# Kernel tuning notes

Hardware: AMD Instinct MI355X
Metric: run time of the kernel (lower is better)

Reference implementation:

```python
import jax, jax.numpy as jnp
import numpy as np

B, N, D = 1, 768, 256
H = 4
HD = D // H
K = 16
EDGE_DIM = 4
LN_EPS = 1e-5


def setup_inputs() -> dict:
    key = jax.random.key(0)
    ks = jax.random.split(key, 16)
    g = lambda k, shape, fan: jax.random.normal(k, shape, jnp.float32) / np.sqrt(fan)
    return {
        'x': jax.random.normal(ks[0], (B, N, D), jnp.float32),
        'Wqkv_w': g(ks[1], (D, 3 * D), D), 'Wqkv_b': jnp.zeros((3 * D,), jnp.float32),
        'out_w': g(ks[2], (D, D), D), 'out_b': jnp.zeros((D,), jnp.float32),
        'ffn1_w': g(ks[3], (2 * D, 2 * D), 2 * D), 'ffn1_b': jnp.zeros((2 * D,), jnp.float32),
        'ln_g': jnp.ones((2 * D,), jnp.float32), 'ln_b': jnp.zeros((2 * D,), jnp.float32),
        'ffn2_w': g(ks[4], (2 * D, D), 2 * D), 'ffn2_b': jnp.zeros((D,), jnp.float32),
        'e1_w': g(ks[5], (EDGE_DIM, 2 * H), EDGE_DIM), 'e1_b': jnp.zeros((2 * H,), jnp.float32),
        'e2_w': g(ks[6], (2 * H, H), 2 * H), 'e2_b': jnp.zeros((H,), jnp.float32),
        'graph_gate': jnp.float32(0.5),
    }


def _normalize(v):
    return v / jnp.clip(jnp.linalg.norm(v, axis=-1, keepdims=True), 1e-12)


def reference(x, Wqkv_w, Wqkv_b, out_w, out_b, ffn1_w, ffn1_b, ln_g, ln_b,
              ffn2_w, ffn2_b, e1_w, e1_b, e2_w, e2_b, graph_gate):
    b, n, d = x.shape
    # ---- graph topology (no grad, discrete top-k) ----
    xs = jax.lax.stop_gradient(x)
    dn_s = _normalize(xs)
    sim_d = jnp.einsum('bnd,bmd->bnm', dn_s, dn_s)
    eye = jnp.eye(n, dtype=bool)
    sim_d = jnp.where(eye, -jnp.inf, sim_d)
    idx = jax.lax.top_k(sim_d, K)[1]                       # (B,N,K)
    adj = jnp.zeros((b, n, n), bool).at[
        jnp.arange(b)[:, None, None], jnp.arange(n)[None, :, None], idx].set(True)
    adj = adj | jnp.swapaxes(adj, 1, 2) | eye              # symmetric + self loops
    # ---- differentiable edge features (B,N,N,4) ----
    dnm = _normalize(x)
    sim = jnp.einsum('bnd,bmd->bnm', dnm, dnm)
    diff = x[:, :, None, :] - x[:, None, :, :]             # (B,N,N,D) memory-bound
    l2 = jnp.linalg.norm(diff, axis=-1) / np.float32(np.sqrt(d))
    ad = jnp.abs(diff)
    ef = jnp.stack([sim, l2, ad.mean(-1), ad.max(-1)], axis=-1)
    # ---- edge bias per head (B,H,N,N) ----
    h = jax.nn.relu(ef @ e1_w + e1_b)
    bias = jnp.transpose(h @ e2_w + e2_b, (0, 3, 1, 2))
    # ---- attention ----
    qkv = (x @ Wqkv_w + Wqkv_b).reshape(b, n, H, HD, 3)
    qkv = jnp.transpose(qkv, (0, 2, 1, 3, 4))              # (B,H,N,HD,3)
    q, k, v = qkv[..., 0], qkv[..., 1], qkv[..., 2]
    logits = jnp.einsum('bhnd,bhmd->bhnm', q, k) / np.float32(np.sqrt(HD))
    logits = logits + graph_gate * bias
    logits = jnp.where(adj[:, None], logits, -jnp.inf)     # sparse masking
    attn = jax.nn.softmax(logits, axis=-1)
    ctx = jnp.einsum('bhnm,bhmd->bhnd', attn, v)
    msg = jnp.transpose(ctx, (0, 2, 1, 3)).reshape(b, n, d) @ out_w + out_b
    # ---- FFN: Linear -> LayerNorm -> GELU -> Linear, residual ----
    y = jnp.concatenate([x, msg], axis=-1) @ ffn1_w + ffn1_b
    mu = y.mean(-1, keepdims=True)
    var = ((y - mu) ** 2).mean(-1, keepdims=True)
    y = (y - mu) / jnp.sqrt(var + LN_EPS) * ln_g + ln_b
    y = jax.nn.gelu(y, approximate=False)
    return x + (y @ ffn2_w + ffn2_b)
```

## Files before the change

### kernel.cpp

```cpp
#include <hip/hip_runtime.h>
#include <hip/hip_bf16.h>
#include <math.h>

#define NN 768
#define DD 256
#define NHEAD 4
#define HDIM 64
#define TOPK 16

typedef __attribute__((ext_vector_type(8))) short short8;
typedef __attribute__((ext_vector_type(4))) float f32x4;

__device__ __forceinline__ unsigned short f2bf(float f) {
    unsigned u = __float_as_uint(f);
    unsigned r = u + 0x7fffu + ((u >> 16) & 1u);
    return (unsigned short)(r >> 16);
}

__global__ __launch_bounds__(256) void k_prep_norms(
        const float* __restrict__ Wqkv, const float* __restrict__ outw,
        const float* __restrict__ f1w,  const float* __restrict__ f2w,
        unsigned short* __restrict__ t_qkv, unsigned short* __restrict__ t_out,
        unsigned short* __restrict__ t_f1,  unsigned short* __restrict__ t_f2,
        const float* __restrict__ x,
        double* __restrict__ nrm2_d, double* __restrict__ nrm_d,
        double* __restrict__ invn_d,
        unsigned short* __restrict__ xb, unsigned int* __restrict__ adjw) {
    int b = blockIdx.x;
    int tid = threadIdx.x;
    if (b < 640) {
        const float* src; unsigned short* dst; int K, C, tile;
        if (b < 192)      { src = Wqkv; dst = t_qkv; K = 256; C = 768; tile = b; }
        else if (b < 256) { src = outw; dst = t_out; K = 256; C = 256; tile = b - 192; }
        else if (b < 512) { src = f1w;  dst = t_f1;  K = 512; C = 512; tile = b - 256; }
        else              { src = f2w;  dst = t_f2;  K = 512; C = 256; tile = b - 512; }
        int tpr = C / 32;
        int k0 = (tile / tpr) * 32, c0 = (tile % tpr) * 32;
        __shared__ float tls[32][33];
        int r = tid >> 3, c4 = (tid & 7) * 4;
        float4 v = *(const float4*)&src[(size_t)(k0 + r) * C + c0 + c4];
        tls[r][c4 + 0] = v.x; tls[r][c4 + 1] = v.y;
        tls[r][c4 + 2] = v.z; tls[r][c4 + 3] = v.w;
        __syncthreads();
        int rc = tid >> 3, k4 = (tid & 7) * 4;
        unsigned short* d = &dst[(size_t)(c0 + rc) * K + k0 + k4];
        d[0] = f2bf(tls[k4 + 0][rc]);
        d[1] = f2bf(tls[k4 + 1][rc]);
        d[2] = f2bf(tls[k4 + 2][rc]);
        d[3] = f2bf(tls[k4 + 3][rc]);
    } else {
        int nb = b - 640;
        int gid = nb * 256 + tid;
        adjw[gid * 3 + 0] = 0u;
        adjw[gid * 3 + 1] = 0u;
        adjw[gid * 3 + 2] = 0u;
        int n = nb * 4 + (tid >> 6);
        int lane = tid & 63;
        const float* row = x + (size_t)n * DD;
        double s = 0.0;
        #pragma unroll
        for (int i = 0; i < 4; ++i) {
            float v = row[lane + 64 * i];
            xb[(size_t)n * DD + lane + 64 * i] = f2bf(v);
            s += (double)v * (double)v;
        }
        for (int off = 32; off > 0; off >>= 1) s += __shfl_down(s, off);
        if (lane == 0) {
            nrm2_d[n] = s;
            double nv = sqrt(s);
            nrm_d[n] = nv;
            invn_d[n] = 1.0 / fmax(nv, 1e-12);
        }
    }
}

__global__ __launch_bounds__(512) void k_simqkv(
        const float* __restrict__ x, const double* __restrict__ invn_d,
        double* __restrict__ simd,
        const unsigned short* __restrict__ xbf,
        const unsigned short* __restrict__ t_qkv,
        const float* __restrict__ Wqkv_b,
        float* __restrict__ qb, float* __restrict__ kb, float* __restrict__ vb) {
    __shared__ float A[2][32][68];
    __shared__ float Bm[2][32][68];
    int b = blockIdx.x;
    int tid = threadIdx.x;
    if (b < 300) {
        int r = (int)((sqrtf(8.f * (float)b + 1.f) - 1.f) * 0.5f);
        while ((r + 1) * (r + 2) / 2 <= b) ++r;
        while (r * (r + 1) / 2 > b) --r;
        int c = b - r * (r + 1) / 2;
        int n0 = c * 32, m0 = r * 32;

        int g = tid >> 8;
        int t = tid & 255;
        int tx = t & 15, ty = t >> 4;
        double d00 = 0.0, d01 = 0.0, d10 = 0.0, d11 = 0.0;

        #pragma unroll
        for (int kt = 0; kt < 2; ++kt) {
            int d0 = g * 128 + kt * 64;
            #pragma unroll
            for (int it = 0; it < 8; ++it) {
                int l = t + 256 * it;
                int rr = l >> 6, cc = l & 63;
                A[g][rr][cc]  = x[(size_t)(n0 + rr) * DD + d0 + cc];
                Bm[g][rr][cc] = x[(size_t)(m0 + rr) * DD + d0 + cc];
            }
            __syncthreads();
            for (int d = 0; d < 64; d += 4) {
                float4 b0 = *(const float4*)&Bm[g][tx][d];
                float4 b1 = *(const float4*)&Bm[g][tx + 16][d];
                float4 a0 = *(const float4*)&A[g][ty][d];
                float4 a1 = *(const float4*)&A[g][ty + 16][d];
                double b0x = b0.x, b0y = b0.y, b0z = b0.z, b0w = b0.w;
                double b1x = b1.x, b1y = b1.y, b1z = b1.z, b1w = b1.w;
                double a0x = a0.x, a0y = a0.y, a0z = a0.z, a0w = a0.w;
                double a1x = a1.x, a1y = a1.y, a1z = a1.z, a1w = a1.w;
                d00 += a0x * b0x + a0y * b0y + a0z * b0z + a0w * b0w;
                d01 += a0x * b1x + a0y * b1y + a0z * b1z + a0w * b1w;
                d10 += a1x * b0x + a1y * b0y + a1z * b0z + a1w * b0w;
                d11 += a1x * b1x + a1y * b1y + a1z * b1z + a1w * b1w;
            }
            __syncthreads();
        }

        double* part = (double*)&A[0][0][0];
        if (g == 1) {
            part[t * 4 + 0] = d00; part[t * 4 + 1] = d01;
            part[t * 4 + 2] = d10; part[t * 4 + 3] = d11;
        }
        __syncthreads();
        if (g == 0) {
            d00 += part[t * 4 + 0]; d01 += part[t * 4 + 1];
            d10 += part[t * 4 + 2]; d11 += part[t * 4 + 3];
            double in_m0 = invn_d[m0 + tx], in_m1 = invn_d[m0 + tx + 16];
            double in_n0 = invn_d[n0 + ty], in_n1 = invn_d[n0 + ty + 16];
            double v00 = d00 * in_n0 * in_m0;
            double v01 = d01 * in_n0 * in_m1;
            double v10 = d10 * in_n1 * in_m0;
            double v11 = d11 * in_n1 * in_m1;
            simd[(size_t)(n0 + ty) * NN + m0 + tx]           = v00;
            simd[(size_t)(n0 + ty) * NN + m0 + tx + 16]      = v01;
            simd[(size_t)(n0 + ty + 16) * NN + m0 + tx]      = v10;
            simd[(size_t)(n0 + ty + 16) * NN + m0 + tx + 16] = v11;
            simd[(size_t)(m0 + tx) * NN + n0 + ty]           = v00;
            simd[(size_t)(m0 + tx + 16) * NN + n0 + ty]      = v01;
            simd[(size_t)(m0 + tx) * NN + n0 + ty + 16]      = v10;
            simd[(size_t)(m0 + tx + 16) * NN + n0 + ty + 16] = v11;
        }
    } else {
        int w = tid >> 6, lane = tid & 63;
        int id = (b - 300) * 8 + w;
        int rt = id % 48, ct = id / 48;
        int m0 = rt * 16, n0 = ct * 16;
        int fr = lane & 15, fg = lane >> 4;
        f32x4 acc = {0.f, 0.f, 0.f, 0.f};
        const unsigned short* brow = &t_qkv[(size_t)(n0 + fr) * DD];
        #pragma unroll
        for (int k0 = 0; k0 < DD; k0 += 32) {
            short8 a = *(const short8*)&xbf[(size_t)(m0 + fr) * DD + k0 + fg * 8];
            short8 bb8 = *(const short8*)&brow[k0 + fg * 8];
            acc = __builtin_amdgcn_mfma_f32_16x16x32_bf16(a, bb8, acc, 0, 0, 0);
        }
        int cidx = n0 + fr;
        int hh = cidx / 192, rem = cidx % 192, hd = rem / 3, s = rem % 3;
        float* dst = (s == 0) ? qb : (s == 1) ? kb : vb;
        float bb = Wqkv_b[cidx];
        #pragma unroll
        for (int r = 0; r < 4; ++r) {
            int n = m0 + fg * 4 + r;
            dst[((size_t)hh * NN + n) * HDIM + hd] = acc[r] + bb;
        }
    }
}

__global__ __launch_bounds__(256) void k_topk(const double* __restrict__ simd,
                                              unsigned char* __restrict__ adj) {
    int n = blockIdx.x;
    int tid = threadIdx.x;
    int w = tid >> 6, l = tid & 63;
    int mbase = w * 192 + l;
    const double* row = simd + (size_t)n * NN;
    double v0 = row[mbase];
    double v1 = row[mbase + 64];
    double v2 = row[mbase + 128];
    if (mbase == n)       v0 = -INFINITY;
    if (mbase + 64 == n)  v1 = -INFINITY;
    if (mbase + 128 == n) v2 = -INFINITY;
    if (tid == 0) adj[(size_t)n * NN + n] = 1;

    __shared__ double wv[2][4];
    __shared__ int    wi[2][4];

    for (int itr = 0; itr < TOPK; ++itr) {
        int p = itr & 1;
        double bv = v0; int bi = mbase;
        if (v1 > bv) { bv = v1; bi = mbase + 64; }
        if (v2 > bv) { bv = v2; bi = mbase + 128; }
        #pragma unroll
        for (int off = 32; off > 0; off >>= 1) {
            double ov = __shfl_down(bv, off);
            int    oi = __shfl_down(bi, off);
            if (ov > bv || (ov == bv && oi < bi)) { bv = ov; bi = oi; }
        }
        if (l == 0) { wv[p][w] = bv; wi[p][w] = bi; }
        __syncthreads();
        double fv = wv[p][0]; int fi = wi[p][0];
        #pragma unroll
        for (int ww = 1; ww < 4; ++ww) {
            double ov = wv[p][ww]; int oi = wi[p][ww];
            if (ov > fv || (ov == fv && oi < fi)) { fv = ov; fi = oi; }
        }
        if (fi == mbase)            v0 = -INFINITY;
        else if (fi == mbase + 64)  v1 = -INFINITY;
        else if (fi == mbase + 128) v2 = -INFINITY;
        if (tid == 0) {
            adj[(size_t)n * NN + fi] = 1;
            adj[(size_t)fi * NN + n] = 1;
        }
    }
}

__global__ __launch_bounds__(256) void k_edge_attn(
        const float* __restrict__ x,
        const double* __restrict__ nrm2_d,
        const double* __restrict__ nrm_d,
        const double* __restrict__ simd,
        const unsigned char* __restrict__ adj,
        const float* __restrict__ e1_w, const float* __restrict__ e1_b,
        const float* __restrict__ e2_w, const float* __restrict__ e2_b,
        const float* __restrict__ gate_p,
        const float* __restrict__ q, const float* __restrict__ k,
        const float* __restrict__ v,
        unsigned short* __restrict__ ctxb) {
    int n = blockIdx.x;
    int tid = threadIdx.x;
    int w = tid >> 6, l = tid & 63;
    __shared__ unsigned short idxs[NN];
    __shared__ float w_sh[NHEAD][NN];
    __shared__ float ef2s[NN];
    __shared__ float ef3s[NN];
    __shared__ float qsh[NHEAD][HDIM];
    __shared__ int wtot[4];

    int c = 0; int loc[3];
    #pragma unroll
    for (int i = 0; i < 3; ++i) {
        int m = 3 * tid + i;
        if (adj[(size_t)n * NN + m]) loc[c++] = m;
    }
    int pc = c;
    #pragma unroll
    for (int off = 1; off < 64; off <<= 1) {
        int o = __shfl_up(pc, off);
        if (l >= off) pc += o;
    }
    if (l == 63) wtot[w] = pc;
    qsh[w][l] = q[((size_t)w * NN + n) * HDIM + l];
    __syncthreads();
    int base = 0;
    #pragma unroll
    for (int ww = 0; ww < 4; ++ww) if (ww < w) base += wtot[ww];
    int start = base + pc - c;
    for (int i = 0; i < c; ++i) idxs[start + i] = (unsigned short)loc[i];
    int cnt = wtot[0] + wtot[1] + wtot[2] + wtot[3];
    __syncthreads();

    float xa[4];
    #pragma unroll
    for (int i = 0; i < 4; ++i) xa[i] = x[(size_t)n * DD + l + 64 * i];

    for (int j = w; j < cnt; j += 4) {
        int m = idxs[j];
        float sab = 0.f, mab = 0.f;
        #pragma unroll
        for (int i = 0; i < 4; ++i) {
            float xb = x[(size_t)m * DD + l + 64 * i];
            float ad = fabsf(xa[i] - xb);
            sab += ad;
            mab = fmaxf(mab, ad);
        }
        #pragma unroll
        for (int off = 32; off > 0; off >>= 1) {
            sab += __shfl_xor(sab, off);
            mab = fmaxf(mab, __shfl_xor(mab, off));
        }
        if (l == 0) { ef2s[j] = sab * (1.f / 256.f); ef3s[j] = mab; }
    }
    __syncthreads();

    double nrm2n = nrm2_d[n];
    double nrmn  = nrm_d[n];
    float gate = gate_p[0];
    for (int j0 = 0; j0 < cnt; j0 += 64) {
        int j = j0 + (tid >> 2);
        int hh = tid & 3;
        if (j < cnt) {
            int m = idxs[j];
            double s_d   = simd[(size_t)n * NN + m];
            double nrm2m = nrm2_d[m];
            double dotd  = s_d * nrmn * nrm_d[m];
            double l2sq  = fmax(nrm2n + nrm2m - 2.0 * dotd, 0.0);
            float ef0 = (float)s_d;
            float ef1 = (float)(sqrt(l2sq) * (1.0 / 16.0));
            float ef2 = ef2s[j];
            float ef3 = ef3s[j];
            float bb = e2_b[hh];
            #pragma unroll
            for (int jj = 0; jj < 8; ++jj) {
                float hv = e1_b[jj] + ef0 * e1_w[0 * 8 + jj] + ef1 * e1_w[1 * 8 + jj]
                         + ef2 * e1_w[2 * 8 + jj] + ef3 * e1_w[3 * 8 + jj];
                bb += fmaxf(hv, 0.f) * e2_w[jj * 4 + hh];
            }
            w_sh[hh][j] = gate * bb;
        }
    }
    __syncthreads();

    int h = w;
    float lmax = -INFINITY;
    for (int j = l; j < cnt; j += 64) {
        int m = idxs[j];
        const float4* kr = (const float4*)(k + ((size_t)h * NN + m) * HDIM);
        float dotv = 0.f;
        #pragma unroll
        for (int d4 = 0; d4 < HDIM / 4; ++d4) {
            float4 kv = kr[d4];
            dotv += qsh[h][4 * d4 + 0] * kv.x + qsh[h][4 * d4 + 1] * kv.y
                  + qsh[h][4 * d4 + 2] * kv.z + qsh[h][4 * d4 + 3] * kv.w;
        }
        w_sh[h][j] = dotv * 0.125f + w_sh[h][j];
        lmax = fmaxf(lmax, w_sh[h][j]);
    }
    #pragma unroll
    for (int off = 32; off > 0; off >>= 1)
        lmax = fmaxf(lmax, __shfl_xor(lmax, off));

    float lsum = 0.f;
    for (int j = l; j < cnt; j += 64) {
        float e = expf(w_sh[h][j] - lmax);
        w_sh[h][j] = e;
        lsum += e;
    }
    #pragma unroll
    for (int off = 32; off > 0; off >>= 1) lsum += __shfl_xor(lsum, off);
    float inv = 1.f / lsum;
    __syncthreads();

    float acc = 0.f;
    #pragma unroll 4
    for (int j = 0; j < cnt; ++j)
        acc += w_sh[h][j] * v[((size_t)h * NN + idxs[j]) * HDIM + l];
    ctxb[(size_t)n * DD + h * HDIM + l] = f2bf(acc * inv);
}

template<int KD, int MODE, bool CONCAT>
__global__ __launch_bounds__(256) void k_gemm_reg(const unsigned short* __restrict__ A,
                                                  const unsigned short* __restrict__ A2,
                                                  const unsigned short* __restrict__ Bt,
                                                  const float* __restrict__ bias,
                                                  const float* __restrict__ resid,
                                                  float* __restrict__ out,
                                                  unsigned short* __restrict__ outb,
                                                  int ncols) {
    int tid = threadIdx.x;
    int w = tid >> 6, lane = tid & 63;
    int m0 = blockIdx.y * 64 + w * 16;
    int n0 = blockIdx.x * 16;
    int fr = lane & 15, fg = lane >> 4;
    f32x4 acc = {0.f, 0.f, 0.f, 0.f};

    const unsigned short* brow = &Bt[(size_t)(n0 + fr) * KD];
    #pragma unroll
    for (int k0 = 0; k0 < KD; k0 += 32) {
        const unsigned short* Asrc = A; int koff = k0;
        if (CONCAT && k0 >= 256) { Asrc = A2; koff = k0 - 256; }
        int lda = CONCAT ? 256 : KD;
        short8 a = *(const short8*)&Asrc[(size_t)(m0 + fr) * lda + koff + fg * 8];
        short8 b = *(const short8*)&brow[k0 + fg * 8];
        acc = __builtin_amdgcn_mfma_f32_16x16x32_bf16(a, b, acc, 0, 0, 0);
    }

    int cidx = n0 + fr;
    float bb = bias[cidx];
    #pragma unroll
    for (int r = 0; r < 4; ++r) {
        int n = m0 + fg * 4 + r;
        float val = acc[r] + bb;
        if (MODE == 1) val += resid[(size_t)n * ncols + cidx];
        if (MODE == 3) outb[(size_t)n * ncols + cidx] = f2bf(val);
        else           out [(size_t)n * ncols + cidx] = val;
    }
}

__global__ __launch_bounds__(256) void k_ln_gelu(const float* __restrict__ y,
                                                 const float* __restrict__ g,
                                                 const float* __restrict__ b,
                                                 unsigned short* __restrict__ ybb) {
    int n = blockIdx.x;
    int tid = threadIdx.x;
    const float* row = y + (size_t)n * 512;
    __shared__ float red[256];
    float v0 = row[tid], v1 = row[tid + 256];

    red[tid] = v0 + v1; __syncthreads();
    for (int s = 128; s > 0; s >>= 1) {
        if (tid < s) red[tid] += red[tid + s];
        __syncthreads();
    }
    float mu = red[0] * (1.f / 512.f);
    __syncthreads();

    float d0 = v0 - mu, d1 = v1 - mu;
    red[tid] = d0 * d0 + d1 * d1; __syncthreads();
    for (int s = 128; s > 0; s >>= 1) {
        if (tid < s) red[tid] += red[tid + s];
        __syncthreads();
    }
    float var = red[0] * (1.f / 512.f);
    float rstd = 1.f / sqrtf(var + 1e-5f);

    float z0 = d0 * rstd * g[tid] + b[tid];
    float z1 = d1 * rstd * g[tid + 256] + b[tid + 256];
    float o0 = 0.5f * z0 * (1.f + erff(z0 * 0.70710678118654752f));
    float o1 = 0.5f * z1 * (1.f + erff(z1 * 0.70710678118654752f));
    ybb[(size_t)n * 512 + tid]       = f2bf(o0);
    ybb[(size_t)n * 512 + tid + 256] = f2bf(o1);
}

extern "C" void kernel_launch(void* const* d_in, const int* in_sizes, int n_in,
                              void* d_out, int out_size, void* d_ws, size_t ws_size,
                              hipStream_t stream) {
    const float* x       = (const float*)d_in[0];
    const float* Wqkv_w  = (const float*)d_in[1];
    const float* Wqkv_b  = (const float*)d_in[2];
    const float* out_w   = (const float*)d_in[3];
    const float* out_b   = (const float*)d_in[4];
    const float* ffn1_w  = (const float*)d_in[5];
    const float* ffn1_b  = (const float*)d_in[6];
    const float* ln_g    = (const float*)d_in[7];
    const float* ln_b    = (const float*)d_in[8];
    const float* ffn2_w  = (const float*)d_in[9];
    const float* ffn2_b  = (const float*)d_in[10];
    const float* e1_w    = (const float*)d_in[11];
    const float* e1_b    = (const float*)d_in[12];
    const float* e2_w    = (const float*)d_in[13];
    const float* e2_b    = (const float*)d_in[14];
    const float* gate    = (const float*)d_in[15];

    char* base = (char*)d_ws;
    double* simd   = (double*)base;            base += (size_t)NN * NN * 8;
    double* nrm2_d = (double*)base;            base += NN * 8;
    double* nrm_d  = (double*)base;            base += NN * 8;
    double* invn_d = (double*)base;            base += NN * 8;
    float* qb      = (float*)base;             base += (size_t)NN * DD * 4;
    float* kb      = (float*)base;             base += (size_t)NN * DD * 4;
    float* vb      = (float*)base;             base += (size_t)NN * DD * 4;
    float* yb      = (float*)base;             base += (size_t)NN * 512 * 4;
    unsigned char* adj = (unsigned char*)base;  base += (size_t)NN * NN;
    unsigned short* xbf  = (unsigned short*)base; base += (size_t)NN * DD * 2;
    unsigned short* ctxb = (unsigned short*)base; base += (size_t)NN * DD * 2;
    unsigned short* msgb = (unsigned short*)base; base += (size_t)NN * DD * 2;
    unsigned short* ybb  = (unsigned short*)base; base += (size_t)NN * 512 * 2;
    unsigned short* t_qkv = (unsigned short*)base; base += (size_t)768 * 256 * 2;
    unsigned short* t_out = (unsigned short*)base; base += (size_t)256 * 256 * 2;
    unsigned short* t_f1  = (unsigned short*)base; base += (size_t)512 * 512 * 2;
    unsigned short* t_f2  = (unsigned short*)base; base += (size_t)256 * 512 * 2;

    k_prep_norms<<<832, 256, 0, stream>>>(Wqkv_w, out_w, ffn1_w, ffn2_w,
                                          t_qkv, t_out, t_f1, t_f2,
                                          x, nrm2_d, nrm_d, invn_d, xbf,
                                          (unsigned int*)adj);

    k_simqkv<<<588, 512, 0, stream>>>(x, invn_d, simd, xbf, t_qkv, Wqkv_b,
                                      qb, kb, vb);

    k_topk<<<NN, 256, 0, stream>>>(simd, adj);

    k_edge_attn<<<NN, 256, 0, stream>>>(x, nrm2_d, nrm_d, simd, adj,
                                        e1_w, e1_b, e2_w, e2_b, gate,
                                        qb, kb, vb, ctxb);

    k_gemm_reg<DD, 3, false><<<dim3(16, 12), 256, 0, stream>>>(
        ctxb, nullptr, t_out, out_b, nullptr, nullptr, msgb, DD);

    k_gemm_reg<512, 0, true><<<dim3(32, 12), 256, 0, stream>>>(
        xbf, msgb, t_f1, ffn1_b, nullptr, yb, nullptr, 512);

    k_ln_gelu<<<NN, 256, 0, stream>>>(yb, ln_g, ln_b, ybb);

    k_gemm_reg<512, 1, false><<<dim3(16, 12), 256, 0, stream>>>(
        ybb, nullptr, t_f2, ffn2_b, x, (float*)d_out, nullptr, DD);
}
```

Before: 78.15 us.

## Fold out-projection into FFN1 weights and use one wave per row in top-k

```diff
diff --git a/kernel.cpp b/kernel.cpp
--- a/kernel.cpp
+++ b/kernel.cpp
@@ -22,6 +22,7 @@
         const float* __restrict__ f1w,  const float* __restrict__ f2w,
         unsigned short* __restrict__ t_qkv, unsigned short* __restrict__ t_out,
         unsigned short* __restrict__ t_f1,  unsigned short* __restrict__ t_f2,
+        unsigned short* __restrict__ t_g,   unsigned short* __restrict__ t_outn,
         const float* __restrict__ x,
         double* __restrict__ nrm2_d, double* __restrict__ nrm_d,
         double* __restrict__ invn_d,
@@ -44,11 +45,16 @@
         __syncthreads();
         int rc = tid >> 3, k4 = (tid & 7) * 4;
         unsigned short* d = &dst[(size_t)(c0 + rc) * K + k0 + k4];
-        d[0] = f2bf(tls[k4 + 0][rc]);
-        d[1] = f2bf(tls[k4 + 1][rc]);
-        d[2] = f2bf(tls[k4 + 2][rc]);
-        d[3] = f2bf(tls[k4 + 3][rc]);
-    } else {
+        unsigned short w0 = f2bf(tls[k4 + 0][rc]);
+        unsigned short w1 = f2bf(tls[k4 + 1][rc]);
+        unsigned short w2 = f2bf(tls[k4 + 2][rc]);
+        unsigned short w3 = f2bf(tls[k4 + 3][rc]);
+        d[0] = w0; d[1] = w1; d[2] = w2; d[3] = w3;
+        if (b >= 256 && b < 512 && k0 < 256) {
+            unsigned short* d2 = &t_g[(size_t)(c0 + rc) * 512 + k0 + k4];
+            d2[0] = w0; d2[1] = w1; d2[2] = w2; d2[3] = w3;
+        }
+    } else if (b < 832) {
         int nb = b - 640;
         int gid = nb * 256 + tid;
         adjw[gid * 3 + 0] = 0u;
@@ -71,6 +77,13 @@
             nrm_d[n] = nv;
             invn_d[n] = 1.0 / fmax(nv, 1e-12);
         }
+    } else {
+        int idx = (b - 832) * 1024 + tid * 4;
+        float4 v = *(const float4*)&outw[idx];
+        t_outn[idx + 0] = f2bf(v.x);
+        t_outn[idx + 1] = f2bf(v.y);
+        t_outn[idx + 2] = f2bf(v.z);
+        t_outn[idx + 3] = f2bf(v.w);
     }
 }
 
@@ -80,7 +93,12 @@
         const unsigned short* __restrict__ xbf,
         const unsigned short* __restrict__ t_qkv,
         const float* __restrict__ Wqkv_b,
-        float* __restrict__ qb, float* __restrict__ kb, float* __restrict__ vb) {
+        float* __restrict__ qb, float* __restrict__ kb, float* __restrict__ vb,
+        const unsigned short* __restrict__ t_f1,
+        const unsigned short* __restrict__ t_outn,
+        unsigned short* __restrict__ t_g,
+        const float* __restrict__ out_b, const float* __restrict__ f1w,
+        const float* __restrict__ ffn1_b, float* __restrict__ bias_f) {
     __shared__ float A[2][32][68];
     __shared__ float Bm[2][32][68];
     int b = blockIdx.x;
@@ -149,7 +167,7 @@
             simd[(size_t)(m0 + tx) * NN + n0 + ty + 16]      = v10;
             simd[(size_t)(m0 + tx + 16) * NN + n0 + ty + 16] = v11;
         }
-    } else {
+    } else if (b < 588) {
         int w = tid >> 6, lane = tid & 63;
         int id = (b - 300) * 8 + w;
         int rt = id % 48, ct = id / 48;
@@ -172,52 +190,67 @@
             int n = m0 + fg * 4 + r;
             dst[((size_t)hh * NN + n) * HDIM + hd] = acc[r] + bb;
         }
+    } else if (b < 652) {
+        int w = tid >> 6, lane = tid & 63;
+        int id = (b - 588) * 8 + w;
+        int m0 = (id & 31) * 16;
+        int n0 = (id >> 5) * 16;
+        int fr = lane & 15, fg = lane >> 4;
+        f32x4 acc = {0.f, 0.f, 0.f, 0.f};
+        const unsigned short* arow = &t_f1[(size_t)(m0 + fr) * 512 + 256];
+        const unsigned short* brow = &t_outn[(size_t)(n0 + fr) * 256];
+        #pragma unroll
+        for (int k0 = 0; k0 < 256; k0 += 32) {
+            short8 a = *(const short8*)&arow[k0 + fg * 8];
+            short8 bb8 = *(const short8*)&brow[k0 + fg * 8];
+            acc = __builtin_amdgcn_mfma_f32_16x16x32_bf16(a, bb8, acc, 0, 0, 0);
+        }
+        #pragma unroll
+        for (int r = 0; r < 4; ++r)
+            t_g[(size_t)(m0 + fg * 4 + r) * 512 + 256 + n0 + fr] = f2bf(acc[r]);
+    } else {
+        float s = ffn1_b[tid];
+        for (int c = 0; c < 256; ++c)
+            s += out_b[c] * f1w[(size_t)(256 + c) * 512 + tid];
+        bias_f[tid] = s;
     }
 }
 
 __global__ __launch_bounds__(256) void k_topk(const double* __restrict__ simd,
                                               unsigned char* __restrict__ adj) {
-    int n = blockIdx.x;
     int tid = threadIdx.x;
     int w = tid >> 6, l = tid & 63;
-    int mbase = w * 192 + l;
+    int n = blockIdx.x * 4 + w;
     const double* row = simd + (size_t)n * NN;
-    double v0 = row[mbase];
-    double v1 = row[mbase + 64];
-    double v2 = row[mbase + 128];
-    if (mbase == n)       v0 = -INFINITY;
-    if (mbase + 64 == n)  v1 = -INFINITY;
-    if (mbase + 128 == n) v2 = -INFINITY;
-    if (tid == 0) adj[(size_t)n * NN + n] = 1;
-
-    __shared__ double wv[2][4];
-    __shared__ int    wi[2][4];
+    double v[12];
+    #pragma unroll
+    for (int i = 0; i < 12; ++i) {
+        int m = l + 64 * i;
+        v[i] = (m == n) ? -INFINITY : row[m];
+    }
+    if (l == 0) adj[(size_t)n * NN + n] = 1;
 
     for (int itr = 0; itr < TOPK; ++itr) {
-        int p = itr & 1;
-        double bv = v0; int bi = mbase;
-        if (v1 > bv) { bv = v1; bi = mbase + 64; }
-        if (v2 > bv) { bv = v2; bi = mbase + 128; }
+        double bv = -INFINITY; int bi = 0x7fffffff;
+        #pragma unroll
+        for (int i = 0; i < 12; ++i) {
+            if (v[i] > bv) { bv = v[i]; bi = l + 64 * i; }
+        }
         #pragma unroll
         for (int off = 32; off > 0; off >>= 1) {
             double ov = __shfl_down(bv, off);
             int    oi = __shfl_down(bi, off);
             if (ov > bv || (ov == bv && oi < bi)) { bv = ov; bi = oi; }
         }
-        if (l == 0) { wv[p][w] = bv; wi[p][w] = bi; }
-        __syncthreads();
-        double fv = wv[p][0]; int fi = wi[p][0];
-        #pragma unroll
-        for (int ww = 1; ww < 4; ++ww) {
-            double ov = wv[p][ww]; int oi = wi[p][ww];
-            if (ov > fv || (ov == fv && oi < fi)) { fv = ov; fi = oi; }
-        }
-        if (fi == mbase)            v0 = -INFINITY;
-        else if (fi == mbase + 64)  v1 = -INFINITY;
-        else if (fi == mbase + 128) v2 = -INFINITY;
-        if (tid == 0) {
-            adj[(size_t)n * NN + fi] = 1;
-            adj[(size_t)fi * NN + n] = 1;
+        bi = __shfl(bi, 0);
+        if ((bi & 63) == l) {
+            int slot = bi >> 6;
+            #pragma unroll
+            for (int i = 0; i < 12; ++i) if (i == slot) v[i] = -INFINITY;
+        }
+        if (l == 0) {
+            adj[(size_t)n * NN + bi] = 1;
+            adj[(size_t)bi * NN + n] = 1;
         }
     }
 }
@@ -461,32 +494,32 @@
     unsigned char* adj = (unsigned char*)base;  base += (size_t)NN * NN;
     unsigned short* xbf  = (unsigned short*)base; base += (size_t)NN * DD * 2;
     unsigned short* ctxb = (unsigned short*)base; base += (size_t)NN * DD * 2;
-    unsigned short* msgb = (unsigned short*)base; base += (size_t)NN * DD * 2;
     unsigned short* ybb  = (unsigned short*)base; base += (size_t)NN * 512 * 2;
     unsigned short* t_qkv = (unsigned short*)base; base += (size_t)768 * 256 * 2;
     unsigned short* t_out = (unsigned short*)base; base += (size_t)256 * 256 * 2;
     unsigned short* t_f1  = (unsigned short*)base; base += (size_t)512 * 512 * 2;
     unsigned short* t_f2  = (unsigned short*)base; base += (size_t)256 * 512 * 2;
-
-    k_prep_norms<<<832, 256, 0, stream>>>(Wqkv_w, out_w, ffn1_w, ffn2_w,
-                                          t_qkv, t_out, t_f1, t_f2,
+    unsigned short* t_g   = (unsigned short*)base; base += (size_t)512 * 512 * 2;
+    unsigned short* t_outn = (unsigned short*)base; base += (size_t)256 * 256 * 2;
+    float* bias_f  = (float*)base;             base += 512 * 4;
+
+    k_prep_norms<<<896, 256, 0, stream>>>(Wqkv_w, out_w, ffn1_w, ffn2_w,
+                                          t_qkv, t_out, t_f1, t_f2, t_g, t_outn,
                                           x, nrm2_d, nrm_d, invn_d, xbf,
                                           (unsigned int*)adj);
 
-    k_simqkv<<<588, 512, 0, stream>>>(x, invn_d, simd, xbf, t_qkv, Wqkv_b,
-                                      qb, kb, vb);
-
-    k_topk<<<NN, 256, 0, stream>>>(simd, adj);
+    k_simqkv<<<653, 512, 0, stream>>>(x, invn_d, simd, xbf, t_qkv, Wqkv_b,
+                                      qb, kb, vb, t_f1, t_outn, t_g,
+                                      out_b, ffn1_w, ffn1_b, bias_f);
+
+    k_topk<<<192, 256, 0, stream>>>(simd, adj);
 
     k_edge_attn<<<NN, 256, 0, stream>>>(x, nrm2_d, nrm_d, simd, adj,
                                         e1_w, e1_b, e2_w, e2_b, gate,
                                         qb, kb, vb, ctxb);
 
-    k_gemm_reg<DD, 3, false><<<dim3(16, 12), 256, 0, stream>>>(
-        ctxb, nullptr, t_out, out_b, nullptr, nullptr, msgb, DD);
-
     k_gemm_reg<512, 0, true><<<dim3(32, 12), 256, 0, stream>>>(
-        xbf, msgb, t_f1, ffn1_b, nullptr, yb, nullptr, 512);
+        xbf, ctxb, t_g, bias_f, nullptr, yb, nullptr, 512);
 
     k_ln_gelu<<<NN, 256, 0, stream>>>(yb, ln_g, ln_b, ybb);
 
```

Measured after the change: 74.05 us. 1.06x faster.
